# Optimization experiments

Measured on AMD Instinct MI355X. Metric: run time of the kernel, lower is better.

## Reference

```python
import jax, jax.numpy as jnp
import numpy as np

B, S, E = 2, 4096, 1024
H = 16
W = 256  # attention_window == chunk size; attn width = 3*W


def _chunk3(x):
    # x: [b, nc, w, h, d] -> stack (prev, cur, next) chunks on last axis: [b, nc, w, h, d, 3]
    prev = jnp.pad(x[:, :-1], ((0, 0), (1, 0), (0, 0), (0, 0), (0, 0)))
    nxt = jnp.pad(x[:, 1:], ((0, 0), (0, 1), (0, 0), (0, 0), (0, 0)))
    return jnp.stack([prev, x, nxt], axis=-1)


def setup_inputs() -> dict:
    key = jax.random.key(0)
    ks = jax.random.split(key, 4)
    hs = jax.random.normal(ks[0], (B, S, E), jnp.float32)

    def lin(k):
        kw, kb = jax.random.split(k)
        return (jax.random.normal(kw, (E, E), jnp.float32) * 0.02,
                jax.random.normal(kb, (E,), jnp.float32) * 0.02)

    Wq, bq = lin(ks[1])
    Wk, bk = lin(ks[2])
    Wv, bv = lin(ks[3])
    return {"hidden_states": hs, "Wq": Wq, "bq": bq, "Wk": Wk, "bk": bk, "Wv": Wv, "bv": bv}


def reference(hidden_states, Wq, bq, Wk, bk, Wv, bv):
    b, s, e = hidden_states.shape
    h, w = H, W
    d = e // h
    nc = s // w  # number of non-overlapping chunks

    # torch nn.Linear: y = x @ W.T + b ; q scaled by 1/sqrt(head_dim)
    q = (hidden_states @ Wq.T + bq) * (1.0 / np.sqrt(d))
    k = hidden_states @ Wk.T + bk
    v = hidden_states @ Wv.T + bv
    q = q.reshape(b, s, h, d)
    k = k.reshape(b, s, h, d)
    v = v.reshape(b, s, h, d)

    # ---- sliding_chunks_no_overlap_matmul_qk ----
    cq = q.reshape(b, nc, w, h, d)
    ck3 = _chunk3(k.reshape(b, nc, w, h, d))  # [b,nc,w,h,d,3]
    # [b,nc,w,h,3,w] -> [b,s,h,3w]
    scores = jnp.einsum('bcxhd,bcyhde->bcxhey', cq, ck3).reshape(b, s, h, 3 * w)

    # ---- mask_invalid_locations (same math as Longformer's helper) ----
    ii = jnp.arange(w)[:, None]
    cc = jnp.arange(w + 1)[None, :]
    beg_mask = cc < (w - ii)   # [w, w+1] applied to first w rows, first w+1 cols
    end_mask = cc >= (w - ii)  # flipped mask, last w rows, last w+1 cols
    neg_inf = jnp.array(-jnp.inf, scores.dtype)
    beg = jnp.where(beg_mask[None, :, None, :], neg_inf, scores[:, :w, :, :w + 1])
    scores = scores.at[:, :w, :, :w + 1].set(beg)
    end = jnp.where(end_mask[None, :, None, :], neg_inf, scores[:, s - w:, :, 3 * w - (w + 1):])
    scores = scores.at[:, s - w:, :, 3 * w - (w + 1):].set(end)

    # softmax in float32 (as in original), cast back
    probs = jax.nn.softmax(scores.astype(jnp.float32), axis=-1).astype(hidden_states.dtype)

    # ---- sliding_chunks_no_overlap_matmul_pv ----
    cp = probs.reshape(b, nc, w, h, 3, w)          # bcwhpd (d = key pos in chunk)
    cv3 = _chunk3(v.reshape(b, nc, w, h, d))       # bcdhep (d = pos, e = head_dim, p = 3)
    attn = jnp.einsum('bcwhpd,bcdhep->bcwhe', cp, cv3).reshape(b, s, h, d)

    return attn.reshape(b, s, e)
```

## Files before the change

### kernel.cpp

```cpp
#include <hip/hip_runtime.h>
#include <math.h>

#define BB  2
#define SS  4096
#define EE  1024
#define HH  16
#define DD  64
#define WW  256
#define NCC 16
#define MTOT (BB*SS)

typedef __attribute__((ext_vector_type(4))) float f32x4;
typedef __attribute__((ext_vector_type(8))) short bf16x8;

__device__ __forceinline__ void gl_lds16(const void* g, void* l) {
  __builtin_amdgcn_global_load_lds(
      (const __attribute__((address_space(1))) unsigned int*)g,
      (__attribute__((address_space(3))) unsigned int*)l,
      16, 0, 0);
}

__device__ __forceinline__ unsigned bf16rne(float f) {
  unsigned u = __float_as_uint(f);
  return (u + (((u >> 16) & 1u) + 0x7fffu)) >> 16;
}

__device__ __forceinline__ unsigned long long pack64(unsigned a, unsigned b,
                                                     unsigned c2, unsigned d) {
  return (unsigned long long)(a | (b << 16)) |
         ((unsigned long long)(c2 | (d << 16)) << 32);
}

__global__ __launch_bounds__(256) void split_all(
    const float* __restrict__ hs, const float* __restrict__ Wq,
    const float* __restrict__ Wk, const float* __restrict__ Wv,
    unsigned short* __restrict__ Ahi, unsigned short* __restrict__ Alo,
    unsigned short* __restrict__ Wqh, unsigned short* __restrict__ Wql,
    unsigned short* __restrict__ Wkh, unsigned short* __restrict__ Wkl,
    unsigned short* __restrict__ Wvh, unsigned short* __restrict__ Wvl)
{
  const int bx = blockIdx.x;
  const float* src; unsigned short *hi, *lo; size_t blk;
  if (bx < 8192)       { src = hs; hi = Ahi; lo = Alo; blk = bx; }
  else if (bx < 9216)  { src = Wq; hi = Wqh; lo = Wql; blk = bx - 8192; }
  else if (bx < 10240) { src = Wk; hi = Wkh; lo = Wkl; blk = bx - 9216; }
  else                 { src = Wv; hi = Wvh; lo = Wvl; blk = bx - 10240; }

  const size_t i = blk * 256 + threadIdx.x;
  const float4 v = ((const float4*)src)[i];
  float f[4] = {v.x, v.y, v.z, v.w};
  unsigned short h[4], l[4];
  #pragma unroll
  for (int j = 0; j < 4; ++j) {
    unsigned u  = __float_as_uint(f[j]);
    unsigned uh = u & 0xFFFF0000u;
    h[j] = (unsigned short)(uh >> 16);
    float r = f[j] - __uint_as_float(uh);
    unsigned ur = __float_as_uint(r);
    ur += ((ur >> 16) & 1u) + 0x7FFFu;
    l[j] = (unsigned short)(ur >> 16);
  }
  *(ushort4*)&hi[4*i] = make_ushort4(h[0], h[1], h[2], h[3]);
  *(ushort4*)&lo[4*i] = make_ushort4(l[0], l[1], l[2], l[3]);
}

struct ProjArgs {
  const unsigned short* Wh;
  const unsigned short* Wl;
  const float* bias;
  unsigned short* outHi;
  unsigned short* outLo;
  float scale;
};

__global__ __launch_bounds__(256) void mfma_proj(
    const unsigned short* __restrict__ Ahi,
    const unsigned short* __restrict__ Alo,
    ProjArgs p0, ProjArgs p1, ProjArgs p2)
{
  __shared__ __align__(16) unsigned short lds[2][4][4096];
  const int tid  = threadIdx.x;
  const int lane = tid & 63;
  const int wid  = tid >> 6;
  const int wr   = wid >> 1, wc = wid & 1;
  const int m0   = blockIdx.x * 128, n0 = blockIdx.y * 128;
  const ProjArgs P = (blockIdx.z == 0) ? p0 : ((blockIdx.z == 1) ? p1 : p2);

  const int q0 = tid, q1 = 256 + tid;
  const int row0 = ((q0 >> 5) << 3) | (q0 & 7), kc0 = (q0 >> 3) & 3;
  const int row1 = ((q1 >> 5) << 3) | (q1 & 7), kc1 = (q1 >> 3) & 3;

  const size_t aoff0 = (size_t)(m0 + row0) * 2048 + (size_t)(kc0 * 16);
  const size_t aoff1 = (size_t)(m0 + row1) * 2048 + (size_t)(kc1 * 16);
  const size_t boff0 = (size_t)(n0 + row0) * 2048 + (size_t)(kc0 * 16);
  const size_t boff1 = (size_t)(n0 + row1) * 2048 + (size_t)(kc1 * 16);

  const int dst0 = (wid * 64) * 16;
  const int dst1 = (256 + wid * 64) * 16;

  const char* gAh = (const char*)Ahi;
  const char* gAl = (const char*)Alo;
  const char* gBh = (const char*)P.Wh;
  const char* gBl = (const char*)P.Wl;

  const int fr = lane & 15;
  const int kc = lane >> 4;
  int a_o[4], b_o[4];
  #pragma unroll
  for (int f = 0; f < 4; ++f) {
    int r = wr * 64 + f * 16 + fr;
    a_o[f] = ((r >> 3) << 9) | (kc << 7) | ((r & 7) << 4);
    r = wc * 64 + f * 16 + fr;
    b_o[f] = ((r >> 3) << 9) | (kc << 7) | ((r & 7) << 4);
  }

  f32x4 acc[4][4];
  #pragma unroll
  for (int i = 0; i < 4; ++i)
    #pragma unroll
    for (int j = 0; j < 4; ++j) acc[i][j] = (f32x4){0.f, 0.f, 0.f, 0.f};

  char* const Lp = (char*)&lds[0][0][0];
  #define PL(b, p) (Lp + (((b)*4 + (p)) * 8192))

  #define STAGE(buf, ks) { const size_t kb = (size_t)(ks) * 64; \
    gl_lds16(gAh + aoff0 + kb, PL(buf,0) + dst0); \
    gl_lds16(gAh + aoff1 + kb, PL(buf,0) + dst1); \
    gl_lds16(gAl + aoff0 + kb, PL(buf,1) + dst0); \
    gl_lds16(gAl + aoff1 + kb, PL(buf,1) + dst1); \
    gl_lds16(gBh + boff0 + kb, PL(buf,2) + dst0); \
    gl_lds16(gBh + boff1 + kb, PL(buf,2) + dst1); \
    gl_lds16(gBl + boff0 + kb, PL(buf,3) + dst0); \
    gl_lds16(gBl + boff1 + kb, PL(buf,3) + dst1); }

  #define COMPUTE(buf) { \
    bf16x8 ah[4], al[4], bh[4], bl[4]; \
    _Pragma("unroll") \
    for (int f = 0; f < 4; ++f) { \
      ah[f] = *(const bf16x8*)(PL(buf,0) + a_o[f]); \
      al[f] = *(const bf16x8*)(PL(buf,1) + a_o[f]); \
      bh[f] = *(const bf16x8*)(PL(buf,2) + b_o[f]); \
      bl[f] = *(const bf16x8*)(PL(buf,3) + b_o[f]); \
    } \
    _Pragma("unroll") \
    for (int i = 0; i < 4; ++i) \
      _Pragma("unroll") \
      for (int j = 0; j < 4; ++j) \
        acc[i][j] = __builtin_amdgcn_mfma_f32_16x16x32_bf16(ah[i], bh[j], acc[i][j], 0,0,0); \
    _Pragma("unroll") \
    for (int i = 0; i < 4; ++i) \
      _Pragma("unroll") \
      for (int j = 0; j < 4; ++j) \
        acc[i][j] = __builtin_amdgcn_mfma_f32_16x16x32_bf16(ah[i], bl[j], acc[i][j], 0,0,0); \
    _Pragma("unroll") \
    for (int i = 0; i < 4; ++i) \
      _Pragma("unroll") \
      for (int j = 0; j < 4; ++j) \
        acc[i][j] = __builtin_amdgcn_mfma_f32_16x16x32_bf16(al[i], bh[j], acc[i][j], 0,0,0); }

  STAGE(0, 0);
  __syncthreads();
  for (int ks = 0; ks < 32; ks += 2) {
    STAGE(1, ks + 1);
    COMPUTE(0);
    __syncthreads();
    if (ks + 2 < 32) STAGE(0, ks + 2);
    COMPUTE(1);
    __syncthreads();
  }
  #undef PL
  #undef STAGE
  #undef COMPUTE

  const int r4 = (lane >> 4) << 2;
  #pragma unroll
  for (int j = 0; j < 4; ++j) {
    const int col = n0 + wc * 64 + j * 16 + fr;
    const float bv = P.bias[col];
    #pragma unroll
    for (int i = 0; i < 4; ++i) {
      const int rrow = m0 + wr * 64 + i * 16 + r4;
      #pragma unroll
      for (int v = 0; v < 4; ++v) {
        const float val = (acc[i][j][v] + bv) * P.scale;
        const unsigned u = __float_as_uint(val);
        const float r = val - __uint_as_float(u & 0xFFFF0000u);
        unsigned ur = __float_as_uint(r);
        ur += ((ur >> 16) & 1u) + 0x7FFFu;
        const size_t o = (size_t)(rrow + v) * EE + col;
        P.outHi[o] = (unsigned short)(u >> 16);
        P.outLo[o] = (unsigned short)(ur >> 16);
      }
    }
  }
}

__global__ __launch_bounds__(256, 2) void attn_mfma(
    const unsigned short* __restrict__ Qh_g, const unsigned short* __restrict__ Ql_g,
    const unsigned short* __restrict__ Kh_g, const unsigned short* __restrict__ Kl_g,
    const unsigned short* __restrict__ Vh_g, const unsigned short* __restrict__ Vl_g,
    float* __restrict__ Og)
{
  __shared__ __align__(16) unsigned short Kf[2][2048];
  __shared__ __align__(16) unsigned short Vt[2][2048];
  __shared__ unsigned long long Pscr[4][256];

  const int c = blockIdx.x, h = blockIdx.y, b = blockIdx.z;
  const int tid = threadIdx.x;
  const int lane = tid & 63, wid = tid >> 6;
  const int g = lane >> 4, lq = lane & 15;

  const size_t qrow0 = (size_t)(b * NCC + c) * WW;
  const int colh = h * DD;

  bf16x8 qfh[4][2], qfl[4][2];
  #pragma unroll
  for (int s = 0; s < 4; ++s)
    #pragma unroll
    for (int ch = 0; ch < 2; ++ch) {
      const size_t off = (qrow0 + wid*64 + s*16 + lq) * EE + colh + ch*32 + g*8;
      qfh[s][ch] = *(const bf16x8*)(Qh_g + off);
      qfl[s][ch] = *(const bf16x8*)(Ql_g + off);
    }

  f32x4 Oa[4][4];
  #pragma unroll
  for (int i = 0; i < 4; ++i)
    #pragma unroll
    for (int j = 0; j < 4; ++j) Oa[i][j] = (f32x4){0.f, 0.f, 0.f, 0.f};
  float m[4], lsum[4];
  #pragma unroll
  for (int s = 0; s < 4; ++s) { m[s] = -1e30f; lsum[s] = 0.f; }

  const int kK = 16*(wid & 1) + lq;
  const int dK = 32*(wid >> 1) + g*8;
  const int stv = tid >> 5, idxv = tid & 31;
  const int kV = 16*(stv >> 2) + (idxv >> 1);
  const int dV = 16*(stv & 3) + 8*(idxv & 1);
  const int C0  = ((dV >> 4) << 6) | ((kV >> 3) << 4) | (dV & 15);
  const int swW = (((dV >> 4) & 1) << 2) | (((kV >> 3) & 1) << 1) | ((dV >> 3) & 1);
  const int vel = kV & 7;

  const long krow0_base = (long)qrow0 - WW;
  const int t0 = (c == 0) ? 8 : 0;
  const int tN = (c == NCC-1) ? 16 : 24;

  uint4 rkh, rkl, rvh, rvl;
  {
    const long kr = krow0_base + (long)t0*32;
    const size_t offK = (size_t)(kr + kK) * EE + colh + dK;
    const size_t offV = (size_t)(kr + kV) * EE + colh + dV;
    rkh = *(const uint4*)(Kh_g + offK); rkl = *(const uint4*)(Kl_g + offK);
    rvh = *(const uint4*)(Vh_g + offV); rvl = *(const uint4*)(Vl_g + offV);
  }

  for (int tt = t0; tt < tN; ++tt) {
    __syncthreads();
    *(uint4*)&Kf[0][wid*512 + lane*8] = rkh;
    *(uint4*)&Kf[1][wid*512 + lane*8] = rkl;
    {
      const unsigned hw[4] = {rvh.x, rvh.y, rvh.z, rvh.w};
      const unsigned lw[4] = {rvl.x, rvl.y, rvl.z, rvl.w};
      #pragma unroll
      for (int t = 0; t < 8; ++t) {
        const int ii = C0*8 + ((t ^ swW) << 3) + vel;
        Vt[0][ii] = (unsigned short)(hw[t >> 1] >> ((t & 1) * 16));
        Vt[1][ii] = (unsigned short)(lw[t >> 1] >> ((t & 1) * 16));
      }
    }
    __syncthreads();

    if (tt + 1 < tN) {
      const long kr = krow0_base + (long)(tt+1)*32;
      const size_t offK = (size_t)(kr + kK) * EE + colh + dK;
      const size_t offV = (size_t)(kr + kV) * EE + colh + dV;
      rkh = *(const uint4*)(Kh_g + offK); rkl = *(const uint4*)(Kl_g + offK);
      rvh = *(const uint4*)(Vh_g + offV); rvl = *(const uint4*)(Vl_g + offV);
    }

    bf16x8 kfh[2][2], kfl[2][2];
    #pragma unroll
    for (int f = 0; f < 4; ++f) {
      const int o = f*512 + lane*8;
      kfh[f & 1][f >> 1] = *(const bf16x8*)&Kf[0][o];
      kfl[f & 1][f >> 1] = *(const bf16x8*)&Kf[1][o];
    }

    bf16x8 vfh[4], vfl[4];
    #pragma unroll
    for (int ds = 0; ds < 4; ++ds) {
      const int rch = ds*64 + g*16 + lq;
      const int rsw = (((rch >> 6) & 1) << 2) | (((rch >> 4) & 1) << 1) | ((rch >> 3) & 1);
      vfh[ds] = *(const bf16x8*)&Vt[0][(rch ^ rsw) * 8];
      vfl[ds] = *(const bf16x8*)&Vt[1][(rch ^ rsw) * 8];
    }

    #pragma unroll
    for (int s = 0; s < 4; ++s) {
      f32x4 ac0 = (f32x4){0.f,0.f,0.f,0.f}, ac1 = (f32x4){0.f,0.f,0.f,0.f};
      #pragma unroll
      for (int ch = 0; ch < 2; ++ch) {
        ac0 = __builtin_amdgcn_mfma_f32_16x16x32_bf16(kfh[0][ch], qfh[s][ch], ac0, 0,0,0);
        ac0 = __builtin_amdgcn_mfma_f32_16x16x32_bf16(kfh[0][ch], qfl[s][ch], ac0, 0,0,0);
        ac0 = __builtin_amdgcn_mfma_f32_16x16x32_bf16(kfl[0][ch], qfh[s][ch], ac0, 0,0,0);
        ac1 = __builtin_amdgcn_mfma_f32_16x16x32_bf16(kfh[1][ch], qfh[s][ch], ac1, 0,0,0);
        ac1 = __builtin_amdgcn_mfma_f32_16x16x32_bf16(kfh[1][ch], qfl[s][ch], ac1, 0,0,0);
        ac1 = __builtin_amdgcn_mfma_f32_16x16x32_bf16(kfl[1][ch], qfh[s][ch], ac1, 0,0,0);
      }

      float tmax = fmaxf(fmaxf(fmaxf(ac0[0],ac0[1]), fmaxf(ac0[2],ac0[3])),
                         fmaxf(fmaxf(ac1[0],ac1[1]), fmaxf(ac1[2],ac1[3])));
      tmax = fmaxf(tmax, __shfl_xor(tmax, 16));
      tmax = fmaxf(tmax, __shfl_xor(tmax, 32));
      const float mo = m[s];
      const float mn = fmaxf(mo, tmax);
      m[s] = mn;
      const float sc = __expf(mo - mn);
      float pv[8];
      #pragma unroll
      for (int r = 0; r < 4; ++r) { pv[r] = __expf(ac0[r] - mn); pv[4+r] = __expf(ac1[r] - mn); }
      float ps = 0.f;
      #pragma unroll
      for (int r = 0; r < 8; ++r) ps += pv[r];
      lsum[s] = lsum[s] * sc + ps;
      #pragma unroll
      for (int ds = 0; ds < 4; ++ds) Oa[ds][s] *= sc;

      unsigned hb[8], lb[8];
      #pragma unroll
      for (int r = 0; r < 8; ++r) {
        hb[r] = bf16rne(pv[r]);
        const float rr = pv[r] - __uint_as_float(hb[r] << 16);
        lb[r] = bf16rne(rr);
      }
      const int pq = (g >> 1)*32 + lq*2 + (g & 1);
      Pscr[wid][pq]            = pack64(hb[0],hb[1],hb[2],hb[3]);
      Pscr[wid][pq + 64]       = pack64(hb[4],hb[5],hb[6],hb[7]);
      Pscr[wid][128 + pq]      = pack64(lb[0],lb[1],lb[2],lb[3]);
      Pscr[wid][128 + pq + 64] = pack64(lb[4],lb[5],lb[6],lb[7]);
      asm volatile("" ::: "memory");
      union U8 { unsigned long long q[2]; bf16x8 v; };
      U8 uh, ul;
      uh.q[0] = Pscr[wid][lane*2];       uh.q[1] = Pscr[wid][lane*2 + 1];
      ul.q[0] = Pscr[wid][128 + lane*2]; ul.q[1] = Pscr[wid][128 + lane*2 + 1];
      const bf16x8 pbh = uh.v;
      const bf16x8 pbl = ul.v;

      #pragma unroll
      for (int ds = 0; ds < 4; ++ds) {
        Oa[ds][s] = __builtin_amdgcn_mfma_f32_16x16x32_bf16(vfh[ds], pbh, Oa[ds][s], 0,0,0);
        Oa[ds][s] = __builtin_amdgcn_mfma_f32_16x16x32_bf16(vfl[ds], pbh, Oa[ds][s], 0,0,0);
        Oa[ds][s] = __builtin_amdgcn_mfma_f32_16x16x32_bf16(vfh[ds], pbl, Oa[ds][s], 0,0,0);
      }
    }
  }

  #pragma unroll
  for (int s = 0; s < 4; ++s) {
    float ls = lsum[s];
    ls += __shfl_xor(ls, 16);
    ls += __shfl_xor(ls, 32);
    const int x = wid*64 + s*16 + lq;
    const float nz = (c == 0) ? (float)x
                   : ((c == NCC-1) ? (float)(WW - 1 - x) : 0.f);
    ls += nz * __expf(0.f - m[s]);
    const float inv = 1.f / ls;
    float* op = Og + (qrow0 + x) * EE + colh;
    #pragma unroll
    for (int ds = 0; ds < 4; ++ds) {
      float4 r;
      r.x = Oa[ds][s][0]*inv; r.y = Oa[ds][s][1]*inv;
      r.z = Oa[ds][s][2]*inv; r.w = Oa[ds][s][3]*inv;
      *(float4*)(op + ds*16 + g*4) = r;
    }
  }
}

extern "C" void kernel_launch(void* const* d_in, const int* in_sizes, int n_in,
                              void* d_out, int out_size, void* d_ws, size_t ws_size,
                              hipStream_t stream) {
    const float* hs = (const float*)d_in[0];
    const float* Wq = (const float*)d_in[1];
    const float* bq = (const float*)d_in[2];
    const float* Wk = (const float*)d_in[3];
    const float* bk = (const float*)d_in[4];
    const float* Wv = (const float*)d_in[5];
    const float* bv = (const float*)d_in[6];
    float* out = (float*)d_out;

    const size_t mat  = (size_t)MTOT * EE;
    const size_t wmat = (size_t)EE * EE;

    unsigned short* w = (unsigned short*)d_ws;
    unsigned short* Ahi = w;            unsigned short* Alo = Ahi + mat;
    unsigned short* Wqh = Alo + mat;    unsigned short* Wql = Wqh + wmat;
    unsigned short* Wkh = Wql + wmat;   unsigned short* Wkl = Wkh + wmat;
    unsigned short* Wvh = Wkl + wmat;   unsigned short* Wvl = Wvh + wmat;
    unsigned short* Qhb = Wvl + wmat;   unsigned short* Qlb = Qhb + mat;
    unsigned short* Khb = Qlb + mat;    unsigned short* Klb = Khb + mat;
    unsigned short* Vhb = Klb + mat;    unsigned short* Vlb = Vhb + mat;

    split_all<<<8192 + 3*1024, 256, 0, stream>>>(
        hs, Wq, Wk, Wv, Ahi, Alo, Wqh, Wql, Wkh, Wkl, Wvh, Wvl);

    ProjArgs pq{Wqh, Wql, bq, Qhb, Qlb, 0.125f};
    ProjArgs pk{Wkh, Wkl, bk, Khb, Klb, 1.0f};
    ProjArgs pv{Wvh, Wvl, bv, Vhb, Vlb, 1.0f};
    dim3 g(MTOT/128, EE/128, 3);
    mfma_proj<<<g, 256, 0, stream>>>(Ahi, Alo, pq, pk, pv);

    dim3 ga(NCC, HH, BB);
    attn_mfma<<<ga, 256, 0, stream>>>(Qhb, Qlb, Khb, Klb, Vhb, Vlb, out);
}
```

Baseline: 351.6 us.

## Enlarge projection GEMM tile to 256x128 with 512 threads and staged epilogue

```diff
diff --git a/kernel.cpp b/kernel.cpp
--- a/kernel.cpp
+++ b/kernel.cpp
@@ -73,30 +73,36 @@
   float scale;
 };
 
-__global__ __launch_bounds__(256) void mfma_proj(
+__global__ __launch_bounds__(512) void mfma_proj(
     const unsigned short* __restrict__ Ahi,
     const unsigned short* __restrict__ Alo,
     ProjArgs p0, ProjArgs p1, ProjArgs p2)
 {
-  __shared__ __align__(16) unsigned short lds[2][4][4096];
+  __shared__ __align__(16) union {
+    unsigned short stage[2][24576];
+    unsigned short ep[128][136];
+  } sh;
+
   const int tid  = threadIdx.x;
   const int lane = tid & 63;
   const int wid  = tid >> 6;
-  const int wr   = wid >> 1, wc = wid & 1;
-  const int m0   = blockIdx.x * 128, n0 = blockIdx.y * 128;
+  const int wr   = wid >> 1;
+  const int wc   = wid & 1;
+  const int m0   = blockIdx.x * 256, n0 = blockIdx.y * 128;
   const ProjArgs P = (blockIdx.z == 0) ? p0 : ((blockIdx.z == 1) ? p1 : p2);
 
-  const int q0 = tid, q1 = 256 + tid;
-  const int row0 = ((q0 >> 5) << 3) | (q0 & 7), kc0 = (q0 >> 3) & 3;
-  const int row1 = ((q1 >> 5) << 3) | (q1 & 7), kc1 = (q1 >> 3) & 3;
-
-  const size_t aoff0 = (size_t)(m0 + row0) * 2048 + (size_t)(kc0 * 16);
-  const size_t aoff1 = (size_t)(m0 + row1) * 2048 + (size_t)(kc1 * 16);
-  const size_t boff0 = (size_t)(n0 + row0) * 2048 + (size_t)(kc0 * 16);
-  const size_t boff1 = (size_t)(n0 + row1) * 2048 + (size_t)(kc1 * 16);
-
-  const int dst0 = (wid * 64) * 16;
-  const int dst1 = (256 + wid * 64) * 16;
+  const int qA0 = tid, qA1 = 512 + tid;
+  const int rowA0 = ((qA0 >> 5) << 3) | (qA0 & 7), kcA0 = (qA0 >> 3) & 3;
+  const int rowA1 = ((qA1 >> 5) << 3) | (qA1 & 7), kcA1 = (qA1 >> 3) & 3;
+  const int rowB  = rowA0, kcB = kcA0;
+
+  const size_t aoff0 = (size_t)(m0 + rowA0) * 2048 + (size_t)(kcA0 * 16);
+  const size_t aoff1 = (size_t)(m0 + rowA1) * 2048 + (size_t)(kcA1 * 16);
+  const size_t boff  = (size_t)(n0 + rowB)  * 2048 + (size_t)(kcB  * 16);
+
+  const int dstA0 = wid * 1024;
+  const int dstA1 = 8192 + wid * 1024;
+  const int dstB  = wid * 1024;
 
   const char* gAh = (const char*)Ahi;
   const char* gAl = (const char*)Alo;
@@ -120,33 +126,42 @@
     #pragma unroll
     for (int j = 0; j < 4; ++j) acc[i][j] = (f32x4){0.f, 0.f, 0.f, 0.f};
 
-  char* const Lp = (char*)&lds[0][0][0];
-  #define PL(b, p) (Lp + (((b)*4 + (p)) * 8192))
+  char* const Lp = (char*)&sh.stage[0][0];
+  #define PL(b, p) (Lp + ((b) * 49152 + (p)))
 
   #define STAGE(buf, ks) { const size_t kb = (size_t)(ks) * 64; \
-    gl_lds16(gAh + aoff0 + kb, PL(buf,0) + dst0); \
-    gl_lds16(gAh + aoff1 + kb, PL(buf,0) + dst1); \
-    gl_lds16(gAl + aoff0 + kb, PL(buf,1) + dst0); \
-    gl_lds16(gAl + aoff1 + kb, PL(buf,1) + dst1); \
-    gl_lds16(gBh + boff0 + kb, PL(buf,2) + dst0); \
-    gl_lds16(gBh + boff1 + kb, PL(buf,2) + dst1); \
-    gl_lds16(gBl + boff0 + kb, PL(buf,3) + dst0); \
-    gl_lds16(gBl + boff1 + kb, PL(buf,3) + dst1); }
+    gl_lds16(gAh + aoff0 + kb, PL(buf,0)     + dstA0); \
+    gl_lds16(gAh + aoff1 + kb, PL(buf,0)     + dstA1); \
+    gl_lds16(gAl + aoff0 + kb, PL(buf,16384) + dstA0); \
+    gl_lds16(gAl + aoff1 + kb, PL(buf,16384) + dstA1); \
+    gl_lds16(gBh + boff  + kb, PL(buf,32768) + dstB); \
+    gl_lds16(gBl + boff  + kb, PL(buf,40960) + dstB); }
 
   #define COMPUTE(buf) { \
-    bf16x8 ah[4], al[4], bh[4], bl[4]; \
+    bf16x8 ah[4], bh[4]; \
     _Pragma("unroll") \
     for (int f = 0; f < 4; ++f) { \
-      ah[f] = *(const bf16x8*)(PL(buf,0) + a_o[f]); \
-      al[f] = *(const bf16x8*)(PL(buf,1) + a_o[f]); \
-      bh[f] = *(const bf16x8*)(PL(buf,2) + b_o[f]); \
-      bl[f] = *(const bf16x8*)(PL(buf,3) + b_o[f]); \
+      ah[f] = *(const bf16x8*)(PL(buf,0)     + a_o[f]); \
+      bh[f] = *(const bf16x8*)(PL(buf,32768) + b_o[f]); \
     } \
+    asm volatile("s_waitcnt lgkmcnt(0)" ::: "memory"); \
+    __builtin_amdgcn_sched_barrier(0); \
+    bf16x8 al[4], bl[4]; \
+    _Pragma("unroll") \
+    for (int f = 0; f < 4; ++f) { \
+      al[f] = *(const bf16x8*)(PL(buf,16384) + a_o[f]); \
+      bl[f] = *(const bf16x8*)(PL(buf,40960) + b_o[f]); \
+    } \
+    __builtin_amdgcn_s_setprio(1); \
     _Pragma("unroll") \
     for (int i = 0; i < 4; ++i) \
       _Pragma("unroll") \
       for (int j = 0; j < 4; ++j) \
         acc[i][j] = __builtin_amdgcn_mfma_f32_16x16x32_bf16(ah[i], bh[j], acc[i][j], 0,0,0); \
+    __builtin_amdgcn_s_setprio(0); \
+    asm volatile("s_waitcnt lgkmcnt(0)" ::: "memory"); \
+    __builtin_amdgcn_sched_barrier(0); \
+    __builtin_amdgcn_s_setprio(1); \
     _Pragma("unroll") \
     for (int i = 0; i < 4; ++i) \
       _Pragma("unroll") \
@@ -156,40 +171,69 @@
     for (int i = 0; i < 4; ++i) \
       _Pragma("unroll") \
       for (int j = 0; j < 4; ++j) \
-        acc[i][j] = __builtin_amdgcn_mfma_f32_16x16x32_bf16(al[i], bh[j], acc[i][j], 0,0,0); }
+        acc[i][j] = __builtin_amdgcn_mfma_f32_16x16x32_bf16(al[i], bh[j], acc[i][j], 0,0,0); \
+    __builtin_amdgcn_s_setprio(0); }
 
   STAGE(0, 0);
-  __syncthreads();
-  for (int ks = 0; ks < 32; ks += 2) {
-    STAGE(1, ks + 1);
-    COMPUTE(0);
-    __syncthreads();
-    if (ks + 2 < 32) STAGE(0, ks + 2);
-    COMPUTE(1);
-    __syncthreads();
-  }
+  STAGE(1, 1);
+  #pragma unroll 2
+  for (int ks = 0; ks < 31; ++ks) {
+    const int b = ks & 1;
+    asm volatile("s_waitcnt vmcnt(6)" ::: "memory");
+    __builtin_amdgcn_sched_barrier(0);
+    __builtin_amdgcn_s_barrier();
+    COMPUTE(b);
+    __builtin_amdgcn_s_barrier();
+    if (ks + 2 < 32) STAGE(b, ks + 2);
+  }
+  asm volatile("s_waitcnt vmcnt(0)" ::: "memory");
+  __builtin_amdgcn_sched_barrier(0);
+  __builtin_amdgcn_s_barrier();
+  COMPUTE(1);
   #undef PL
   #undef STAGE
   #undef COMPUTE
 
   const int r4 = (lane >> 4) << 2;
   #pragma unroll
-  for (int j = 0; j < 4; ++j) {
-    const int col = n0 + wc * 64 + j * 16 + fr;
-    const float bv = P.bias[col];
-    #pragma unroll
-    for (int i = 0; i < 4; ++i) {
-      const int rrow = m0 + wr * 64 + i * 16 + r4;
-      #pragma unroll
-      for (int v = 0; v < 4; ++v) {
-        const float val = (acc[i][j][v] + bv) * P.scale;
-        const unsigned u = __float_as_uint(val);
-        const float r = val - __uint_as_float(u & 0xFFFF0000u);
-        unsigned ur = __float_as_uint(r);
-        ur += ((ur >> 16) & 1u) + 0x7FFFu;
-        const size_t o = (size_t)(rrow + v) * EE + col;
-        P.outHi[o] = (unsigned short)(u >> 16);
-        P.outLo[o] = (unsigned short)(ur >> 16);
+  for (int hh = 0; hh < 2; ++hh) {
+    #pragma unroll
+    for (int plane = 0; plane < 2; ++plane) {
+      __syncthreads();
+      if ((wr >> 1) == hh) {
+        #pragma unroll
+        for (int j = 0; j < 4; ++j) {
+          const int col_l = wc*64 + j*16 + fr;
+          const float bv = P.bias[n0 + col_l];
+          #pragma unroll
+          for (int i = 0; i < 4; ++i) {
+            const int rl0 = (wr & 1)*64 + i*16 + r4;
+            #pragma unroll
+            for (int v = 0; v < 4; ++v) {
+              const float val = (acc[i][j][v] + bv) * P.scale;
+              const unsigned u = __float_as_uint(val);
+              unsigned sv;
+              if (plane == 0) { sv = u >> 16; }
+              else {
+                const float rres = val - __uint_as_float(u & 0xFFFF0000u);
+                unsigned ur = __float_as_uint(rres);
+                ur += ((ur >> 16) & 1u) + 0x7FFFu; sv = ur >> 16;
+              }
+              const int rl = rl0 + v;
+              sh.ep[rl][(((col_l >> 3) ^ (rl & 7)) << 3) + (col_l & 7)] =
+                  (unsigned short)sv;
+            }
+          }
+        }
+      }
+      __syncthreads();
+      unsigned short* const OUT = plane ? P.outLo : P.outHi;
+      #pragma unroll
+      for (int u2 = 0; u2 < 4; ++u2) {
+        const int chunk = u2 * 512 + tid;
+        const int rr = chunk >> 4, c16 = chunk & 15;
+        const bf16x8 vv = *(const bf16x8*)&sh.ep[rr][(c16 ^ (rr & 7)) << 3];
+        *(bf16x8*)&OUT[(size_t)(m0 + hh*128 + rr) * EE + n0 + c16*8] = vv;
       }
     }
   }
@@ -406,8 +450,8 @@
     ProjArgs pq{Wqh, Wql, bq, Qhb, Qlb, 0.125f};
     ProjArgs pk{Wkh, Wkl, bk, Khb, Klb, 1.0f};
     ProjArgs pv{Wvh, Wvl, bv, Vhb, Vlb, 1.0f};
-    dim3 g(MTOT/128, EE/128, 3);
-    mfma_proj<<<g, 256, 0, stream>>>(Ahi, Alo, pq, pk, pv);
+    dim3 g(MTOT/256, EE/128, 3);
+    mfma_proj<<<g, 512, 0, stream>>>(Ahi, Alo, pq, pk, pv);
 
     dim3 ga(NCC, HH, BB);
     attn_mfma<<<ga, 256, 0, stream>>>(Qhb, Qlb, Khb, Klb, Vhb, Vlb, out);
```

Measured after the change: 316.3 us. 1.11x faster.
